# Kernel tuning notes

Hardware: AMD Instinct MI355X
Metric: run time of the kernel (lower is better)

The kernel has to match this reference:

```python
import jax, jax.numpy as jnp
import numpy as np

N_NODES = 100000
N_EDGES = 1600000
D_IN = 64
D_HID = 64
D_OUT = 64


def sage_conv(x, src, dst, W_l, W_r, b, n_nodes):
    # PyG SAGEConv (aggr='mean'): out = lin_l(mean_{j in N(i)} x_j) + lin_r(x_i)
    msg = x[src]                                   # [E, d] gather (irregular)
    agg = jax.ops.segment_sum(msg, dst, num_segments=n_nodes)   # [N, d]
    cnt = jax.ops.segment_sum(jnp.ones((src.shape[0], 1), x.dtype), dst,
                              num_segments=n_nodes)             # [N, 1]
    mean = agg / jnp.maximum(cnt, 1.0)
    return mean @ W_l + x @ W_r + b


def setup_inputs() -> dict:
    key = jax.random.key(0)
    k_x, k_e, k1, k2, k3, k4 = jax.random.split(key, 6)
    x = jax.random.normal(k_x, (N_NODES, D_IN), dtype=jnp.float32)
    edge_index = jax.random.randint(k_e, (2, N_EDGES), 0, N_NODES, dtype=jnp.int64)
    s = 1.0 / np.sqrt(D_IN)
    W_l1 = jax.random.uniform(k1, (D_IN, D_HID), jnp.float32, -s, s)
    W_r1 = jax.random.uniform(k2, (D_IN, D_HID), jnp.float32, -s, s)
    b1 = jnp.zeros((D_HID,), jnp.float32)
    s2 = 1.0 / np.sqrt(D_HID)
    W_l2 = jax.random.uniform(k3, (D_HID, D_OUT), jnp.float32, -s2, s2)
    W_r2 = jax.random.uniform(k4, (D_HID, D_OUT), jnp.float32, -s2, s2)
    b2 = jnp.zeros((D_OUT,), jnp.float32)
    return {"x": x, "edge_index": edge_index,
            "W_l1": W_l1, "W_r1": W_r1, "b1": b1,
            "W_l2": W_l2, "W_r2": W_r2, "b2": b2}


def reference(x, edge_index, W_l1, W_r1, b1, W_l2, W_r2, b2):
    src, dst = edge_index[0], edge_index[1]
    n = x.shape[0]
    h = sage_conv(x, src, dst, W_l1, W_r1, b1, n)
    h = jax.nn.relu(h)
    # dropout is identity in eval mode (training=False)
    out = sage_conv(h, src, dst, W_l2, W_r2, b2, n)
    return out
```

## Files before the change

kernel.cpp:

```cpp
#include <hip/hip_runtime.h>

#define DFEAT 64
#define SBSH 10
#define SBN 1024
#define NSB 98
#define ETILE 4096
#define PACKSH 17
#define SRCMASK 0x1FFFF

typedef __bf16 bf16x8 __attribute__((ext_vector_type(8)));
typedef float f32x4 __attribute__((ext_vector_type(4)));

__device__ __forceinline__ unsigned bf16_rne(float v) {
    unsigned bits = __float_as_uint(v);
    return (bits + 0x7FFFu + ((bits >> 16) & 1u)) >> 16;
}
__device__ __forceinline__ float lo16(unsigned u) { return __uint_as_float(u << 16); }
__device__ __forceinline__ float hi16(unsigned u) { return __uint_as_float(u & 0xFFFF0000u); }

__global__ __launch_bounds__(512) void setup_kernel(
    const int* __restrict__ dst, int n_edges, int nt, int* __restrict__ counts,
    const float* __restrict__ x, unsigned short* __restrict__ xb, int ncvt,
    const float* __restrict__ Wl1, const float* __restrict__ Wr1,
    const float* __restrict__ Wl2, const float* __restrict__ Wr2,
    unsigned short* __restrict__ wpack) {
    int b = blockIdx.x, t = threadIdx.x;
    if (b < nt) {
        __shared__ int lh[NSB];
        if (t < NSB) lh[t] = 0;
        __syncthreads();
        int s0 = b * ETILE;
        int s1 = s0 + ETILE; if (s1 > n_edges) s1 = n_edges;
        for (int e = s0 + t; e < s1; e += 512)
            atomicAdd(&lh[dst[e] >> SBSH], 1);
        __syncthreads();
        if (t < NSB) counts[t * nt + b] = lh[t];
    } else if (b < nt + 4) {
        int u = (b - nt) * 512 + t;
        int l = u & 63;
        int ct = (u >> 6) & 3;
        int chunk = (u >> 8) & 1;
        int gemm = (u >> 9) & 1;
        int layer = (u >> 10) & 1;
        const float* W = layer ? (gemm ? Wr2 : Wl2) : (gemm ? Wr1 : Wl1);
        int col = ct * 16 + (l & 15);
        int k0 = chunk * 32 + (l >> 4) * 8;
        unsigned hi[8], lo[8];
#pragma unroll
        for (int j = 0; j < 8; ++j) {
            float w = W[(k0 + j) * DFEAT + col];
            unsigned h = bf16_rne(w);
            float whi = __uint_as_float(h << 16);
            lo[j] = bf16_rne(w - whi);
            hi[j] = h;
        }
        size_t fh = ((((size_t)(layer * 2 + gemm) * 2 + 0) * 2 + chunk) * 4 + ct) * 64 + l;
        size_t fl = ((((size_t)(layer * 2 + gemm) * 2 + 1) * 2 + chunk) * 4 + ct) * 64 + l;
        int4 vh, vl;
        vh.x = hi[0] | (hi[1] << 16); vh.y = hi[2] | (hi[3] << 16);
        vh.z = hi[4] | (hi[5] << 16); vh.w = hi[6] | (hi[7] << 16);
        vl.x = lo[0] | (lo[1] << 16); vl.y = lo[2] | (lo[3] << 16);
        vl.z = lo[4] | (lo[5] << 16); vl.w = lo[6] | (lo[7] << 16);
        ((int4*)wpack)[fh] = vh;
        ((int4*)wpack)[fl] = vl;
    } else {
        int i = (b - nt - 4) * 512 + t;
        if (i < ncvt) {
            const float4* xp = (const float4*)x;
            float4 a = xp[2 * i], c = xp[2 * i + 1];
            int4 o;
            o.x = bf16_rne(a.x) | (bf16_rne(a.y) << 16);
            o.y = bf16_rne(a.z) | (bf16_rne(a.w) << 16);
            o.z = bf16_rne(c.x) | (bf16_rne(c.y) << 16);
            o.w = bf16_rne(c.z) | (bf16_rne(c.w) << 16);
            ((int4*)xb)[i] = o;
        }
    }
}

__global__ __launch_bounds__(512) void tscan1_kernel(const int* __restrict__ counts,
                                                     int nt,
                                                     int* __restrict__ tilebase,
                                                     int* __restrict__ sbtot) {
    __shared__ int sdata[512];
    int sb = blockIdx.x, t = threadIdx.x;
    int v = (t < nt) ? counts[sb * nt + t] : 0;
    sdata[t] = v;
    __syncthreads();
    for (int off = 1; off < 512; off <<= 1) {
        int x = (t >= off) ? sdata[t - off] : 0;
        __syncthreads();
        sdata[t] += x;
        __syncthreads();
    }
    if (t < nt) tilebase[sb * nt + t] = sdata[t] - v;
    if (t == 511) sbtot[sb] = sdata[511];
}

__global__ __launch_bounds__(128) void tscan2_kernel(const int* __restrict__ sbtot,
                                                     int* __restrict__ sbbase,
                                                     int n_edges) {
    __shared__ int sdata[128];
    int t = threadIdx.x;
    int v = (t < NSB) ? sbtot[t] : 0;
    sdata[t] = v;
    __syncthreads();
    for (int off = 1; off < 128; off <<= 1) {
        int x = (t >= off) ? sdata[t - off] : 0;
        __syncthreads();
        sdata[t] += x;
        __syncthreads();
    }
    if (t < NSB) sbbase[t] = sdata[t] - v;
    if (t == 0) sbbase[NSB] = n_edges;
}

__global__ __launch_bounds__(512) void partition_kernel(const int* __restrict__ src,
                                                        const int* __restrict__ dst,
                                                        int n_edges, int nt,
                                                        const int* __restrict__ tilebase,
                                                        const int* __restrict__ sbbase,
                                                        int* __restrict__ tmp) {
    __shared__ int lcur[NSB];
    int t = threadIdx.x;
    if (t < NSB) lcur[t] = sbbase[t] + tilebase[t * nt + blockIdx.x];
    __syncthreads();
    int s0 = blockIdx.x * ETILE;
    int s1 = s0 + ETILE; if (s1 > n_edges) s1 = n_edges;
    for (int e = s0 + t; e < s1; e += 512) {
        int d = dst[e];
        int sb = d >> SBSH;
        int ofs = atomicAdd(&lcur[sb], 1);
        tmp[ofs] = ((d & (SBN - 1)) << PACKSH) | src[e];
    }
}

__global__ __launch_bounds__(1024) void bucket_sort_kernel(
    const int* __restrict__ sbbase, const int* __restrict__ tmp,
    int* __restrict__ col_src, int* __restrict__ row_ptr,
    int n_nodes, int n_edges) {
    __shared__ int cnt[SBN];
    __shared__ int scan[SBN];
    int b = blockIdx.x, t = threadIdx.x;
    int gb = sbbase[b], ge = sbbase[b + 1];
    cnt[t] = 0;
    __syncthreads();
    for (int e = gb + t; e < ge; e += 1024)
        atomicAdd(&cnt[((unsigned)tmp[e]) >> PACKSH], 1);
    __syncthreads();
    int v = cnt[t];
    scan[t] = v;
    __syncthreads();
    for (int off = 1; off < 1024; off <<= 1) {
        int x = (t >= off) ? scan[t - off] : 0;
        __syncthreads();
        scan[t] += x;
        __syncthreads();
    }
    int excl = scan[t] - v;
    int node = (b << SBSH) + t;
    if (node < n_nodes) row_ptr[node] = gb + excl;
    cnt[t] = gb + excl;
    if (b == (int)gridDim.x - 1 && t == 0) row_ptr[n_nodes] = n_edges;
    __syncthreads();
    for (int e = gb + t; e < ge; e += 1024) {
        int pk = tmp[e];
        int pos = atomicAdd(&cnt[((unsigned)pk) >> PACKSH], 1);
        col_src[pos] = (pk & SRCMASK) << 7;
    }
}

template <bool RELU, bool OUT_BF16>
__global__ __launch_bounds__(512, 4) void sage_kernel(
    const int* __restrict__ row_ptr, const int* __restrict__ col_src,
    const unsigned short* __restrict__ xb,
    const unsigned short* __restrict__ wpk,
    const float* __restrict__ bias, void* __restrict__ outp, int n_nodes) {
    __shared__ unsigned short sMean[16 * 72];
    int t = threadIdx.x;
    int w = t >> 6;
    int lane = t & 63;
    int g4 = lane >> 4;
    int p4 = lane & 15;
    int node0 = blockIdx.x * 16;
    const char* xb8 = (const char*)xb + p4 * 8;

    int nA = node0 + w;
    int nB = node0 + w + 8;
    int ncA = nA < n_nodes ? nA : n_nodes - 1;
    int ncB = nB < n_nodes ? nB : n_nodes - 1;
    int baseA = row_ptr[ncA], endA = row_ptr[ncA + 1];
    int baseB = row_ptr[ncB], endB = row_ptr[ncB + 1];
    int degA = endA - baseA, degB = endB - baseB;

    float accA[4] = {0.f, 0.f, 0.f, 0.f};
    float accB[4] = {0.f, 0.f, 0.f, 0.f};

    while (baseA < endA || baseB < endB) {
        int mA = endA - baseA; if (mA > 64) mA = 64; if (mA < 0) mA = 0;
        int mB = endB - baseB; if (mB > 64) mB = 64; if (mB < 0) mB = 0;
        int soffA = mA > 0 ? col_src[baseA + (lane < mA ? lane : 0)] : 0;
        int soffB = mB > 0 ? col_src[baseB + (lane < mB ? lane : 0)] : 0;
        int mmax = mA > mB ? mA : mB;
        for (int i = 0; i < mmax; i += 16) {
#pragma unroll
            for (int k = 0; k < 4; ++k) {
                int base4 = i + 4 * k;
                int n = base4 + g4;
                if (base4 < mA) {
                    int off = __shfl(soffA, n < mA ? n : 0);
                    float f = (n < mA) ? 1.f : 0.f;
                    int2 v = *(const int2*)(xb8 + off);
                    accA[0] += f * lo16((unsigned)v.x);
                    accA[1] += f * hi16((unsigned)v.x);
                    accA[2] += f * lo16((unsigned)v.y);
                    accA[3] += f * hi16((unsigned)v.y);
                }
                if (base4 < mB) {
                    int off = __shfl(soffB, n < mB ? n : 0);
                    float f = (n < mB) ? 1.f : 0.f;
                    int2 v = *(const int2*)(xb8 + off);
                    accB[0] += f * lo16((unsigned)v.x);
                    accB[1] += f * hi16((unsigned)v.x);
                    accB[2] += f * lo16((unsigned)v.y);
                    accB[3] += f * hi16((unsigned)v.y);
                }
            }
        }
        baseA += 64;
        baseB += 64;
    }

#pragma unroll
    for (int e = 0; e < 4; ++e) {
        accA[e] += __shfl_xor(accA[e], 16); accA[e] += __shfl_xor(accA[e], 32);
        accB[e] += __shfl_xor(accB[e], 16); accB[e] += __shfl_xor(accB[e], 32);
    }

    if (g4 == 0) {
        float invA = degA > 0 ? 1.f / (float)degA : 0.f;
        float invB = degB > 0 ? 1.f / (float)degB : 0.f;
        int2 oA, oB;
        oA.x = bf16_rne(accA[0] * invA) | (bf16_rne(accA[1] * invA) << 16);
        oA.y = bf16_rne(accA[2] * invA) | (bf16_rne(accA[3] * invA) << 16);
        oB.x = bf16_rne(accB[0] * invB) | (bf16_rne(accB[1] * invB) << 16);
        oB.y = bf16_rne(accB[2] * invB) | (bf16_rne(accB[3] * invB) << 16);
        *(int2*)&sMean[w * 72 + p4 * 4] = oA;
        *(int2*)&sMean[(w + 8) * 72 + p4 * 4] = oB;
    }
    __syncthreads();

    if (w < 4) {
        int ct = w;
        int row16 = lane & 15;
        int kq = lane >> 4;
        bf16x8 aA0 = *(const bf16x8*)&sMean[row16 * 72 + kq * 8];
        bf16x8 aA1 = *(const bf16x8*)&sMean[row16 * 72 + 32 + kq * 8];
        int xr = node0 + row16; if (xr >= n_nodes) xr = n_nodes - 1;
        const char* xp = (const char*)xb + (size_t)xr * 128 + kq * 16;
        bf16x8 aX0 = *(const bf16x8*)xp;
        bf16x8 aX1 = *(const bf16x8*)(xp + 64);

        const bf16x8* wp = (const bf16x8*)wpk;
        float bcol = bias[ct * 16 + row16];
        f32x4 acc = {bcol, bcol, bcol, bcol};
        acc = __builtin_amdgcn_mfma_f32_16x16x32_bf16(aA0, wp[0 * 256 + ct * 64 + lane], acc, 0, 0, 0);
        acc = __builtin_amdgcn_mfma_f32_16x16x32_bf16(aA1, wp[1 * 256 + ct * 64 + lane], acc, 0, 0, 0);
        acc = __builtin_amdgcn_mfma_f32_16x16x32_bf16(aA0, wp[2 * 256 + ct * 64 + lane], acc, 0, 0, 0);
        acc = __builtin_amdgcn_mfma_f32_16x16x32_bf16(aA1, wp[3 * 256 + ct * 64 + lane], acc, 0, 0, 0);
        acc = __builtin_amdgcn_mfma_f32_16x16x32_bf16(aX0, wp[4 * 256 + ct * 64 + lane], acc, 0, 0, 0);
        acc = __builtin_amdgcn_mfma_f32_16x16x32_bf16(aX1, wp[5 * 256 + ct * 64 + lane], acc, 0, 0, 0);
        acc = __builtin_amdgcn_mfma_f32_16x16x32_bf16(aX0, wp[6 * 256 + ct * 64 + lane], acc, 0, 0, 0);
        acc = __builtin_amdgcn_mfma_f32_16x16x32_bf16(aX1, wp[7 * 256 + ct * 64 + lane], acc, 0, 0, 0);
#pragma unroll
        for (int reg = 0; reg < 4; ++reg) {
            int row = kq * 4 + reg;
            int gn = node0 + row;
            if (gn < n_nodes) {
                float v = acc[reg];
                if (RELU) v = fmaxf(v, 0.0f);
                if (OUT_BF16) {
                    ((unsigned short*)outp)[(size_t)gn * DFEAT + ct * 16 + row16] =
                        (unsigned short)bf16_rne(v);
                } else {
                    ((float*)outp)[(size_t)gn * DFEAT + ct * 16 + row16] = v;
                }
            }
        }
    }
}

extern "C" void kernel_launch(void* const* d_in, const int* in_sizes, int n_in,
                              void* d_out, int out_size, void* d_ws, size_t ws_size,
                              hipStream_t stream) {
    const float* x   = (const float*)d_in[0];
    const int*   ei  = (const int*)d_in[1];
    const float* Wl1 = (const float*)d_in[2];
    const float* Wr1 = (const float*)d_in[3];
    const float* b1  = (const float*)d_in[4];
    const float* Wl2 = (const float*)d_in[5];
    const float* Wr2 = (const float*)d_in[6];
    const float* b2  = (const float*)d_in[7];
    float* out = (float*)d_out;

    int n_nodes = in_sizes[0] / DFEAT;
    int n_edges = in_sizes[1] / 2;
    const int* src  = ei;
    const int* dstv = ei + n_edges;
    int nt = (n_edges + ETILE - 1) / ETILE;

    auto align = [](size_t v) { return (v + 255) & ~(size_t)255; };
    char* ws = (char*)d_ws;
    int* counts   = (int*)ws;            ws += align((size_t)NSB * nt * 4);
    int* tilebase = (int*)ws;            ws += align((size_t)NSB * nt * 4);
    int* sbtot    = (int*)ws;            ws += align(NSB * 4);
    int* sbbase   = (int*)ws;            ws += align((NSB + 1) * 4);
    int* row_ptr  = (int*)ws;            ws += align(((size_t)n_nodes + 1) * 4);
    int* col_src  = (int*)ws;            ws += align((size_t)n_edges * 4);
    unsigned short* xb    = (unsigned short*)ws; ws += align((size_t)n_nodes * DFEAT * 2);
    unsigned short* hb    = (unsigned short*)ws; ws += align((size_t)n_nodes * DFEAT * 2);
    unsigned short* wpack = (unsigned short*)ws; ws += align((size_t)32768);
    int* tmp      = (int*)d_out;

    int ncvt = n_nodes * DFEAT / 8;
    int cvtb = (ncvt + 511) / 512;
    setup_kernel<<<nt + 4 + cvtb, 512, 0, stream>>>(dstv, n_edges, nt, counts,
                                                    x, xb, ncvt,
                                                    Wl1, Wr1, Wl2, Wr2, wpack);
    tscan1_kernel<<<NSB, 512, 0, stream>>>(counts, nt, tilebase, sbtot);
    tscan2_kernel<<<1, 128, 0, stream>>>(sbtot, sbbase, n_edges);
    partition_kernel<<<nt, 512, 0, stream>>>(src, dstv, n_edges, nt, tilebase,
                                             sbbase, tmp);
    bucket_sort_kernel<<<NSB, 1024, 0, stream>>>(sbbase, tmp, col_src, row_ptr,
                                                 n_nodes, n_edges);

    int tiles = (n_nodes + 15) / 16;
    sage_kernel<true, true><<<tiles, 512, 0, stream>>>(row_ptr, col_src, xb,
                                                       wpack, b1, hb, n_nodes);
    sage_kernel<false, false><<<tiles, 512, 0, stream>>>(row_ptr, col_src, hb,
                                                         wpack + 2048 * 8, b2,
                                                         out, n_nodes);
}
```

Measured before the change: 151.5 us.

## Use 32-node tiles with dynamic per-warp node-pair scheduling in SAGE kernel

Each block now covers 32 nodes instead of 16. Warps pull node pairs from a shared atomic counter, so warps that draw low-degree nodes take more work and degree imbalance inside a block evens out. All 8 warps now do MFMA (two 16-row tiles × 4 column tiles) instead of only 4. A branch-free fast path for full groups of four neighbors drops the mask multiply, the shared-memory stride changes to 68, and the launch bounds ask for 8 waves per SIMD, which limits registers and may cause spills. The price is a shared atomic per pair and more register pressure.

```diff
diff --git a/kernel.cpp b/kernel.cpp
--- a/kernel.cpp
+++ b/kernel.cpp
@@ -7,6 +7,7 @@
 #define ETILE 4096
 #define PACKSH 17
 #define SRCMASK 0x1FFFF
+#define MSTRIDE 68
 
 typedef __bf16 bf16x8 __attribute__((ext_vector_type(8)));
 typedef float f32x4 __attribute__((ext_vector_type(4)));
@@ -171,91 +172,118 @@
 }
 
 template <bool RELU, bool OUT_BF16>
-__global__ __launch_bounds__(512, 4) void sage_kernel(
+__global__ __launch_bounds__(512, 8) void sage_kernel(
     const int* __restrict__ row_ptr, const int* __restrict__ col_src,
     const unsigned short* __restrict__ xb,
     const unsigned short* __restrict__ wpk,
     const float* __restrict__ bias, void* __restrict__ outp, int n_nodes) {
-    __shared__ unsigned short sMean[16 * 72];
+    __shared__ unsigned short sMean[32 * MSTRIDE];
+    __shared__ int qcnt;
     int t = threadIdx.x;
     int w = t >> 6;
     int lane = t & 63;
     int g4 = lane >> 4;
     int p4 = lane & 15;
-    int node0 = blockIdx.x * 16;
+    int tile32 = blockIdx.x * 32;
     const char* xb8 = (const char*)xb + p4 * 8;
-
-    int nA = node0 + w;
-    int nB = node0 + w + 8;
-    int ncA = nA < n_nodes ? nA : n_nodes - 1;
-    int ncB = nB < n_nodes ? nB : n_nodes - 1;
-    int baseA = row_ptr[ncA], endA = row_ptr[ncA + 1];
-    int baseB = row_ptr[ncB], endB = row_ptr[ncB + 1];
-    int degA = endA - baseA, degB = endB - baseB;
-
-    float accA[4] = {0.f, 0.f, 0.f, 0.f};
-    float accB[4] = {0.f, 0.f, 0.f, 0.f};
-
-    while (baseA < endA || baseB < endB) {
-        int mA = endA - baseA; if (mA > 64) mA = 64; if (mA < 0) mA = 0;
-        int mB = endB - baseB; if (mB > 64) mB = 64; if (mB < 0) mB = 0;
-        int soffA = mA > 0 ? col_src[baseA + (lane < mA ? lane : 0)] : 0;
-        int soffB = mB > 0 ? col_src[baseB + (lane < mB ? lane : 0)] : 0;
-        int mmax = mA > mB ? mA : mB;
-        for (int i = 0; i < mmax; i += 16) {
+    if (t == 0) qcnt = 0;
+    __syncthreads();
+
+    for (;;) {
+        int pairIdx;
+        if (lane == 0) pairIdx = atomicAdd(&qcnt, 1);
+        pairIdx = __shfl(pairIdx, 0);
+        if (pairIdx >= 16) break;
+        int rowA = pairIdx * 2;
+        int rowB = rowA + 1;
+        int nA = tile32 + rowA;
+        int nB = tile32 + rowB;
+        int ncA = nA < n_nodes ? nA : n_nodes - 1;
+        int ncB = nB < n_nodes ? nB : n_nodes - 1;
+        int baseA = row_ptr[ncA], endA = row_ptr[ncA + 1];
+        int baseB = row_ptr[ncB], endB = row_ptr[ncB + 1];
+        int degA = endA - baseA, degB = endB - baseB;
+
+        float accA[4] = {0.f, 0.f, 0.f, 0.f};
+        float accB[4] = {0.f, 0.f, 0.f, 0.f};
+        while (baseA < endA || baseB < endB) {
+            int mA = endA - baseA; mA = mA > 64 ? 64 : (mA < 0 ? 0 : mA);
+            int mB = endB - baseB; mB = mB > 64 ? 64 : (mB < 0 ? 0 : mB);
+            int soffA = mA > 0 ? col_src[baseA + (lane < mA ? lane : 0)] : 0;
+            int soffB = mB > 0 ? col_src[baseB + (lane < mB ? lane : 0)] : 0;
+            int mmax = mA > mB ? mA : mB;
+            for (int i = 0; i < mmax; i += 16) {
 #pragma unroll
-            for (int k = 0; k < 4; ++k) {
-                int base4 = i + 4 * k;
-                int n = base4 + g4;
-                if (base4 < mA) {
-                    int off = __shfl(soffA, n < mA ? n : 0);
-                    float f = (n < mA) ? 1.f : 0.f;
-                    int2 v = *(const int2*)(xb8 + off);
-                    accA[0] += f * lo16((unsigned)v.x);
-                    accA[1] += f * hi16((unsigned)v.x);
-                    accA[2] += f * lo16((unsigned)v.y);
-                    accA[3] += f * hi16((unsigned)v.y);
-                }
-                if (base4 < mB) {
-                    int off = __shfl(soffB, n < mB ? n : 0);
-                    float f = (n < mB) ? 1.f : 0.f;
-                    int2 v = *(const int2*)(xb8 + off);
-                    accB[0] += f * lo16((unsigned)v.x);
-                    accB[1] += f * hi16((unsigned)v.x);
-                    accB[2] += f * lo16((unsigned)v.y);
-                    accB[3] += f * hi16((unsigned)v.y);
+                for (int k = 0; k < 4; ++k) {
+                    int s4 = i + 4 * k;
+                    int n = s4 + g4;
+                    if (s4 + 4 <= mA) {
+                        int off = __shfl(soffA, n);
+                        int2 v = *(const int2*)(xb8 + off);
+                        accA[0] += lo16((unsigned)v.x);
+                        accA[1] += hi16((unsigned)v.x);
+                        accA[2] += lo16((unsigned)v.y);
+                        accA[3] += hi16((unsigned)v.y);
+                    } else if (s4 < mA) {
+                        int off = __shfl(soffA, n < mA ? n : 0);
+                        float f = (n < mA) ? 1.f : 0.f;
+                        int2 v = *(const int2*)(xb8 + off);
+                        accA[0] += f * lo16((unsigned)v.x);
+                        accA[1] += f * hi16((unsigned)v.x);
+                        accA[2] += f * lo16((unsigned)v.y);
+                        accA[3] += f * hi16((unsigned)v.y);
+                    }
+                    if (s4 + 4 <= mB) {
+                        int off = __shfl(soffB, n);
+                        int2 v = *(const int2*)(xb8 + off);
+                        accB[0] += lo16((unsigned)v.x);
+                        accB[1] += hi16((unsigned)v.x);
+                        accB[2] += lo16((unsigned)v.y);
+                        accB[3] += hi16((unsigned)v.y);
+                    } else if (s4 < mB) {
+                        int off = __shfl(soffB, n < mB ? n : 0);
+                        float f = (n < mB) ? 1.f : 0.f;
+                        int2 v = *(const int2*)(xb8 + off);
+                        accB[0] += f * lo16((unsigned)v.x);
+                        accB[1] += f * hi16((unsigned)v.x);
+                        accB[2] += f * lo16((unsigned)v.y);
+                        accB[3] += f * hi16((unsigned)v.y);
+                    }
                 }
             }
-        }
-        baseA += 64;
-        baseB += 64;
-    }
+            baseA += 64;
+            baseB += 64;
+        }
 
 #pragma unroll
-    for (int e = 0; e < 4; ++e) {
-        accA[e] += __shfl_xor(accA[e], 16); accA[e] += __shfl_xor(accA[e], 32);
-        accB[e] += __shfl_xor(accB[e], 16); accB[e] += __shfl_xor(accB[e], 32);
-    }
-
-    if (g4 == 0) {
-        float invA = degA > 0 ? 1.f / (float)degA : 0.f;
-        float invB = degB > 0 ? 1.f / (float)degB : 0.f;
-        int2 oA, oB;
-        oA.x = bf16_rne(accA[0] * invA) | (bf16_rne(accA[1] * invA) << 16);
-        oA.y = bf16_rne(accA[2] * invA) | (bf16_rne(accA[3] * invA) << 16);
-        oB.x = bf16_rne(accB[0] * invB) | (bf16_rne(accB[1] * invB) << 16);
-        oB.y = bf16_rne(accB[2] * invB) | (bf16_rne(accB[3] * invB) << 16);
-        *(int2*)&sMean[w * 72 + p4 * 4] = oA;
-        *(int2*)&sMean[(w + 8) * 72 + p4 * 4] = oB;
-    }
-    __syncthreads();
-
-    if (w < 4) {
-        int ct = w;
+        for (int e = 0; e < 4; ++e) {
+            accA[e] += __shfl_xor(accA[e], 16); accA[e] += __shfl_xor(accA[e], 32);
+            accB[e] += __shfl_xor(accB[e], 16); accB[e] += __shfl_xor(accB[e], 32);
+        }
+
+        if (g4 == 0) {
+            float invA = degA > 0 ? 1.f / (float)degA : 0.f;
+            float invB = degB > 0 ? 1.f / (float)degB : 0.f;
+            int2 oA, oB;
+            oA.x = bf16_rne(accA[0] * invA) | (bf16_rne(accA[1] * invA) << 16);
+            oA.y = bf16_rne(accA[2] * invA) | (bf16_rne(accA[3] * invA) << 16);
+            oB.x = bf16_rne(accB[0] * invB) | (bf16_rne(accB[1] * invB) << 16);
+            oB.y = bf16_rne(accB[2] * invB) | (bf16_rne(accB[3] * invB) << 16);
+            *(int2*)&sMean[rowA * MSTRIDE + p4 * 4] = oA;
+            *(int2*)&sMean[rowB * MSTRIDE + p4 * 4] = oB;
+        }
+    }
+    __syncthreads();
+
+    {
+        int tile = w >> 2;
+        int ct = w & 3;
         int row16 = lane & 15;
         int kq = lane >> 4;
-        bf16x8 aA0 = *(const bf16x8*)&sMean[row16 * 72 + kq * 8];
-        bf16x8 aA1 = *(const bf16x8*)&sMean[row16 * 72 + 32 + kq * 8];
+        int node0 = tile32 + tile * 16;
+        int srow = tile * 16 + row16;
+        bf16x8 aA0 = *(const bf16x8*)&sMean[srow * MSTRIDE + kq * 8];
+        bf16x8 aA1 = *(const bf16x8*)&sMean[srow * MSTRIDE + 32 + kq * 8];
         int xr = node0 + row16; if (xr >= n_nodes) xr = n_nodes - 1;
         const char* xp = (const char*)xb + (size_t)xr * 128 + kq * 16;
         bf16x8 aX0 = *(const bf16x8*)xp;
@@ -263,21 +291,21 @@
 
         const bf16x8* wp = (const bf16x8*)wpk;
         float bcol = bias[ct * 16 + row16];
-        f32x4 acc = {bcol, bcol, bcol, bcol};
-        acc = __builtin_amdgcn_mfma_f32_16x16x32_bf16(aA0, wp[0 * 256 + ct * 64 + lane], acc, 0, 0, 0);
-        acc = __builtin_amdgcn_mfma_f32_16x16x32_bf16(aA1, wp[1 * 256 + ct * 64 + lane], acc, 0, 0, 0);
-        acc = __builtin_amdgcn_mfma_f32_16x16x32_bf16(aA0, wp[2 * 256 + ct * 64 + lane], acc, 0, 0, 0);
-        acc = __builtin_amdgcn_mfma_f32_16x16x32_bf16(aA1, wp[3 * 256 + ct * 64 + lane], acc, 0, 0, 0);
-        acc = __builtin_amdgcn_mfma_f32_16x16x32_bf16(aX0, wp[4 * 256 + ct * 64 + lane], acc, 0, 0, 0);
-        acc = __builtin_amdgcn_mfma_f32_16x16x32_bf16(aX1, wp[5 * 256 + ct * 64 + lane], acc, 0, 0, 0);
-        acc = __builtin_amdgcn_mfma_f32_16x16x32_bf16(aX0, wp[6 * 256 + ct * 64 + lane], acc, 0, 0, 0);
-        acc = __builtin_amdgcn_mfma_f32_16x16x32_bf16(aX1, wp[7 * 256 + ct * 64 + lane], acc, 0, 0, 0);
+        f32x4 acc2 = {bcol, bcol, bcol, bcol};
+        acc2 = __builtin_amdgcn_mfma_f32_16x16x32_bf16(aA0, wp[0 * 256 + ct * 64 + lane], acc2, 0, 0, 0);
+        acc2 = __builtin_amdgcn_mfma_f32_16x16x32_bf16(aA1, wp[1 * 256 + ct * 64 + lane], acc2, 0, 0, 0);
+        acc2 = __builtin_amdgcn_mfma_f32_16x16x32_bf16(aA0, wp[2 * 256 + ct * 64 + lane], acc2, 0, 0, 0);
+        acc2 = __builtin_amdgcn_mfma_f32_16x16x32_bf16(aA1, wp[3 * 256 + ct * 64 + lane], acc2, 0, 0, 0);
+        acc2 = __builtin_amdgcn_mfma_f32_16x16x32_bf16(aX0, wp[4 * 256 + ct * 64 + lane], acc2, 0, 0, 0);
+        acc2 = __builtin_amdgcn_mfma_f32_16x16x32_bf16(aX1, wp[5 * 256 + ct * 64 + lane], acc2, 0, 0, 0);
+        acc2 = __builtin_amdgcn_mfma_f32_16x16x32_bf16(aX0, wp[6 * 256 + ct * 64 + lane], acc2, 0, 0, 0);
+        acc2 = __builtin_amdgcn_mfma_f32_16x16x32_bf16(aX1, wp[7 * 256 + ct * 64 + lane], acc2, 0, 0, 0);
 #pragma unroll
         for (int reg = 0; reg < 4; ++reg) {
             int row = kq * 4 + reg;
             int gn = node0 + row;
             if (gn < n_nodes) {
-                float v = acc[reg];
+                float v = acc2[reg];
                 if (RELU) v = fmaxf(v, 0.0f);
                 if (OUT_BF16) {
                     ((unsigned short*)outp)[(size_t)gn * DFEAT + ct * 16 + row16] =
@@ -334,7 +362,7 @@
     bucket_sort_kernel<<<NSB, 1024, 0, stream>>>(sbbase, tmp, col_src, row_ptr,
                                                  n_nodes, n_edges);
 
-    int tiles = (n_nodes + 15) / 16;
+    int tiles = (n_nodes + 31) / 32;
     sage_kernel<true, true><<<tiles, 512, 0, stream>>>(row_ptr, col_src, xb,
                                                        wpack, b1, hb, n_nodes);
     sage_kernel<false, false><<<tiles, 512, 0, stream>>>(row_ptr, col_src, hb,
```

Result: slower. 169.0 us (+11.6%).
